# Optimization experiments

Measured on AMD Instinct MI355X. Metric: run time of the kernel, lower is better.

The kernel has to match this reference:

```python
import jax, jax.numpy as jnp
import numpy as np

N = 100_000   # nodes
E = 3_200_000 # edges (avg degree 32)
IN = 256      # input feature dim


def setup_inputs() -> dict:
    key = jax.random.key(0)
    ks = jax.random.split(key, 10)
    w = lambda k, s: (jax.random.normal(k, s, jnp.float32) * 0.02)
    return {
        "x": jax.random.normal(ks[0], (N, IN), jnp.float32),
        "edge_index": jax.random.randint(ks[1], (2, E), 0, N, dtype=jnp.int32),
        "edge_attr": jax.random.normal(ks[2], (E, 1), jnp.float32),
        # conv1: ExpGraphConv(IN, 64, 128)
        "W1a": w(ks[3], (IN, 64)), "b1a": jnp.zeros((64,), jnp.float32),
        "W1b": w(ks[4], (IN + 64, 128)), "b1b": jnp.zeros((128,), jnp.float32),
        # conv2: ExpGraphConv(128, 32->hidden 64? per ctor (128, 32, 64)): msg hidden 32... kept as repo: hidden=32? Using (128,64) msg, (192,64) out per faithful cat structure
        "W2a": w(ks[5], (128, 64)), "b2a": jnp.zeros((64,), jnp.float32),
        "W2b": w(ks[6], (128 + 64, 64)), "b2b": jnp.zeros((64,), jnp.float32),
        # head
        "Wl1": w(ks[7], (64, 32)), "bl1": jnp.zeros((32,), jnp.float32),
        "Wl2": w(ks[8], (32, 1)), "bl2": jnp.zeros((1,), jnp.float32),
    }


def _mean_aggr(h, src, dst, n):
    # gather messages from source nodes, scatter-mean into destination nodes
    s = jax.ops.segment_sum(h[src], dst, num_segments=n)          # [N, d]
    cnt = jax.ops.segment_sum(jnp.ones((src.shape[0],), h.dtype), dst, num_segments=n)
    return s / jnp.maximum(cnt, 1.0)[:, None]


def _exp_graph_conv(x, src, dst, Wa, ba, Wb, bb):
    # message MLP on source features, mean aggregation, then linear on [x || aggr]
    h = x @ Wa + ba                                               # [N, hidden]
    m = _mean_aggr(h, src, dst, x.shape[0])                       # [N, hidden]
    return jnp.concatenate([x, m], axis=1) @ Wb + bb              # [N, out]


def reference(x, edge_index, edge_attr, W1a, b1a, W1b, b1b, W2a, b2a, W2b, b2b, Wl1, bl1, Wl2, bl2):
    src, dst = edge_index[0], edge_index[1]
    x = jax.nn.relu(_exp_graph_conv(x, src, dst, W1a, b1a, W1b, b1b))
    x = jax.nn.relu(_exp_graph_conv(x, src, dst, W2a, b2a, W2b, b2b))
    x = jax.nn.relu(x @ Wl1 + bl1)
    return x @ Wl2 + bl2
```

## Files before the change

### kernel.cpp

```cpp
#include <hip/hip_runtime.h>

#define IN_DIM 256
#define CAP 10240
#define EPB 4096

typedef _Float16 f16;
typedef _Float16 f16x8 __attribute__((ext_vector_type(8)));
typedef float f32x4 __attribute__((ext_vector_type(4)));
typedef unsigned u32x4 __attribute__((ext_vector_type(4)));
typedef unsigned u32x2 __attribute__((ext_vector_type(2)));


__global__ __launch_bounds__(256) void bucket_scatter_k(const int* __restrict__ srcp,
                                                        const int* __restrict__ dstp,
                                                        int* __restrict__ bcur,
                                                        unsigned* __restrict__ bedge, int E) {
    __shared__ int cnt[512], lstart[512], delta[512], fill[512];
    __shared__ int pfx[256];
    __shared__ unsigned spay[EPB];
    __shared__ unsigned char sbk[EPB];
    int tid = threadIdx.x;
    cnt[tid] = 0; cnt[tid + 256] = 0;
    fill[tid] = 0; fill[tid + 256] = 0;
    __syncthreads();
    size_t base = (size_t)blockIdx.x * EPB;
    int nloc = E - (int)base; if (nloc > EPB) nloc = EPB;
    int dreg[EPB / 256], sreg[EPB / 256];
#pragma unroll
    for (int j = 0; j < EPB / 256; j++) {
        int e = j * 256 + tid;
        if (e < nloc) {
            dreg[j] = dstp[base + e];
            sreg[j] = srcp[base + e];
            atomicAdd(&cnt[dreg[j] >> 8], 1);
        }
    }
    __syncthreads();
    int a0 = cnt[2 * tid], a1 = cnt[2 * tid + 1], s = a0 + a1;
    pfx[tid] = s;
    __syncthreads();
    for (int off = 1; off < 256; off <<= 1) {
        int t2 = (tid >= off) ? pfx[tid - off] : 0;
        __syncthreads();
        pfx[tid] += t2;
        __syncthreads();
    }
    int excl = pfx[tid] - s;
    lstart[2 * tid] = excl;
    lstart[2 * tid + 1] = excl + a0;
    int g0 = 0, g1 = 0;
    if (a0) g0 = atomicAdd(&bcur[2 * tid], a0);
    if (a1) g1 = atomicAdd(&bcur[2 * tid + 1], a1);
    delta[2 * tid]     = (2 * tid) * CAP + g0 - excl;
    delta[2 * tid + 1] = (2 * tid + 1) * CAP + g1 - (excl + a0);
    __syncthreads();
#pragma unroll
    for (int j = 0; j < EPB / 256; j++) {
        int e = j * 256 + tid;
        if (e < nloc) {
            int d = dreg[j], bk = d >> 8;
            int slot = lstart[bk] + atomicAdd(&fill[bk], 1);
            spay[slot] = (unsigned)sreg[j] | ((unsigned)(d & 255) << 17);
            sbk[slot] = (unsigned char)bk;
        }
    }
    __syncthreads();
    int mid = lstart[256];
#pragma unroll
    for (int j = 0; j < EPB / 256; j++) {
        int i = j * 256 + tid;
        if (i < nloc) {
            int bk = (int)sbk[i] | ((i >= mid) ? 256 : 0);
            int gp = i + delta[bk];
            if (gp < (bk + 1) * CAP)
                bedge[gp] = spay[i];
        }
    }
}

__global__ __launch_bounds__(256) void fine_sort_k(unsigned* __restrict__ bedge,
                                                   const int* __restrict__ bcur,
                                                   int2* __restrict__ ose, int Nn) {
    __shared__ int cnt[256], cur[256], pfx[256];
    __shared__ int sorted[CAP];
    int b = blockIdx.x, tid = threadIdx.x;
    int lo = b * CAP;
    int sz = bcur[b];
    if (sz > CAP) sz = CAP;
    cnt[tid] = 0;
    __syncthreads();
    for (int i = tid; i < sz; i += 256) atomicAdd(&cnt[bedge[lo + i] >> 17], 1);
    __syncthreads();
    int c = cnt[tid];
    pfx[tid] = c;
    __syncthreads();
    for (int off = 1; off < 256; off <<= 1) {
        int t2 = (tid >= off) ? pfx[tid - off] : 0;
        __syncthreads();
        pfx[tid] += t2;
        __syncthreads();
    }
    int excl = pfx[tid] - c;
    cur[tid] = excl;
    int node = b * 256 + tid;
    if (node < Nn) ose[node] = make_int2(lo + excl, lo + excl + c);
    __syncthreads();
    for (int i = tid; i < sz; i += 256) {
        unsigned v = bedge[lo + i];
        int slot = atomicAdd(&cur[v >> 17], 1);
        sorted[slot] = (int)(v & 0x1FFFFu);
    }
    __syncthreads();
    for (int i = tid; i < sz; i += 256) bedge[lo + i] = (unsigned)sorted[i];
}


__global__ __launch_bounds__(256) void wcast_all_k(
    const float* __restrict__ W1a, const float* __restrict__ W1b,
    const float* __restrict__ W2a, const float* __restrict__ W2b,
    const float* __restrict__ b1a, const float* __restrict__ b1b,
    const float* __restrict__ b2a, const float* __restrict__ b2b,
    f16* __restrict__ Wt1, f16* __restrict__ Wt2,
    f16* __restrict__ Wmt1, f16* __restrict__ Wmt2,
    float* __restrict__ bc1, float* __restrict__ bc2) {
    int i = blockIdx.x * 256 + threadIdx.x;
    if (i < 49152) {
        int n = i >> 8, k = i & 255;
        Wt1[i] = (f16)(n < 64 ? W1a[k * 64 + n] : W1b[k * 128 + (n - 64)]);
    } else if (i < 65536) {
        int l = i - 49152; int n = l >> 7, k = l & 127;
        Wt2[l] = (f16)(n < 64 ? W2a[k * 64 + n] : W2b[k * 64 + (n - 64)]);
    } else if (i < 73728) {
        int l = i - 65536; int n = l >> 6, k = l & 63;
        Wmt1[l] = (f16)W1b[(256 + k) * 128 + n];
    } else if (i < 77824) {
        int l = i - 73728; int n = l >> 6, k = l & 63;
        Wmt2[l] = (f16)W2b[(128 + k) * 64 + n];
    } else if (i < 78016) {
        int l = i - 77824; bc1[l] = l < 64 ? b1a[l] : b1b[l - 64];
    } else if (i < 78144) {
        int l = i - 78016; bc2[l] = l < 64 ? b2a[l] : b2b[l - 64];
    }
}


template <int BN, bool A1F32>
__global__ __launch_bounds__(256) void gemm_fused(const void* __restrict__ A1v, int K1,
                                                  const f16* __restrict__ Wt,
                                                  const float* __restrict__ bc,
                                                  f16* __restrict__ Y1,
                                                  f16* __restrict__ Y2, int M) {
    constexpr int BM = 64, BK = 32, ASTR = BK + 8;
    constexpr int WN = BN / 2, NB = WN / 16, SEGB = BN / 64;
    constexpr int EPS = BN + 8, TPR = BN / 8, N2 = BN - 64;
    constexpr size_t SM_AB = (size_t)BM * ASTR * 2 + (size_t)BN * ASTR * 2;
    constexpr size_t SM_EP = (size_t)BM * EPS * 2;
    constexpr size_t SM = SM_AB > SM_EP ? SM_AB : SM_EP;
    __shared__ __align__(16) char smem[SM];
    f16* As = reinterpret_cast<f16*>(smem);
    f16* Bs = reinterpret_cast<f16*>(smem + (size_t)BM * ASTR * 2);
    const int tid  = threadIdx.x;
    const int wave = tid >> 6, lane = tid & 63;
    const int wr = wave >> 1, wc = wave & 1;
    const int quad = lane >> 4, l16 = lane & 15;
    const int row0 = blockIdx.x * BM;

    f32x4 acc[2][NB];
#pragma unroll
    for (int i = 0; i < 2; i++)
#pragma unroll
        for (int j = 0; j < NB; j++) acc[i][j] = (f32x4)(0.f);

    const int ra = tid >> 2, sa = tid & 3;
    int rowA = row0 + ra;  if (rowA >= M) rowA = M - 1;

    u32x4 aReg, bReg[SEGB];
    auto loadA = [&](int kk) {
        if constexpr (A1F32) {
            const float* bp = reinterpret_cast<const float*>(A1v) +
                              (size_t)rowA * K1 + kk + sa * 8;
            f32x4 v0 = __builtin_nontemporal_load(reinterpret_cast<const f32x4*>(bp));
            f32x4 v1 = __builtin_nontemporal_load(reinterpret_cast<const f32x4*>(bp) + 1);
            union { f16 h[8]; u32x4 u; } p;
            p.h[0] = (f16)v0.x; p.h[1] = (f16)v0.y; p.h[2] = (f16)v0.z; p.h[3] = (f16)v0.w;
            p.h[4] = (f16)v1.x; p.h[5] = (f16)v1.y; p.h[6] = (f16)v1.z; p.h[7] = (f16)v1.w;
            aReg = p.u;
        } else {
            aReg = __builtin_nontemporal_load(reinterpret_cast<const u32x4*>(
                reinterpret_cast<const f16*>(A1v) + (size_t)rowA * K1 + kk + sa * 8));
        }
    };
    auto loadB = [&](int kk) {
#pragma unroll
        for (int i = 0; i < SEGB; i++) {
            int fid = tid + i * 256;
            int n = fid >> 2, s = fid & 3;
            bReg[i] = *reinterpret_cast<const u32x4*>(Wt + (size_t)n * K1 + kk + s * 8);
        }
    };

    loadA(0); loadB(0);
    for (int kk = 0; kk < K1; kk += BK) {
        *reinterpret_cast<u32x4*>(&As[ra * ASTR + sa * 8]) = aReg;
#pragma unroll
        for (int i = 0; i < SEGB; i++) {
            int fid = tid + i * 256;
            int n = fid >> 2, s = fid & 3;
            *reinterpret_cast<u32x4*>(&Bs[n * ASTR + s * 8]) = bReg[i];
        }
        __syncthreads();
        if (kk + BK < K1) { loadA(kk + BK); loadB(kk + BK); }
        f16x8 af[2], bf[NB];
#pragma unroll
        for (int rb = 0; rb < 2; rb++) {
            int row = wr * 32 + rb * 16 + l16;
            af[rb] = *reinterpret_cast<const f16x8*>(&As[row * ASTR + quad * 8]);
        }
#pragma unroll
        for (int cb = 0; cb < NB; cb++) {
            int n = wc * WN + cb * 16 + l16;
            bf[cb] = *reinterpret_cast<const f16x8*>(&Bs[n * ASTR + quad * 8]);
        }
#pragma unroll
        for (int rb = 0; rb < 2; rb++)
#pragma unroll
            for (int cb = 0; cb < NB; cb++)
                acc[rb][cb] = __builtin_amdgcn_mfma_f32_16x16x32_f16(af[rb], bf[cb], acc[rb][cb], 0, 0, 0);
        __syncthreads();
    }

    f16* ep = reinterpret_cast<f16*>(smem);
#pragma unroll
    for (int rb = 0; rb < 2; rb++) {
#pragma unroll
        for (int cb = 0; cb < NB; cb++) {
            int col = wc * WN + cb * 16 + l16;
            float bv = bc[col];
#pragma unroll
            for (int r = 0; r < 4; r++) {
                int lrow = wr * 32 + rb * 16 + quad * 4 + r;
                ep[(size_t)lrow * EPS + col] = (f16)(acc[rb][cb][r] + bv);
            }
        }
    }
    __syncthreads();
#pragma unroll
    for (int p = 0; p < BM * TPR / 256; p++) {
        int fid = p * 256 + tid;
        int row = fid / TPR, c = fid % TPR, col0 = c * 8;
        int grow = row0 + row;
        if (grow < M) {
            u32x4 val = *reinterpret_cast<const u32x4*>(&ep[(size_t)row * EPS + col0]);
            if (col0 < 64)
                *reinterpret_cast<u32x4*>(Y1 + (size_t)grow * 64 + col0) = val;
            else
                __builtin_nontemporal_store(val,
                    reinterpret_cast<u32x4*>(Y2 + (size_t)grow * N2 + (col0 - 64)));
        }
    }
}


__global__ __launch_bounds__(256) void aggr_k(const int2* __restrict__ ose,
                                              const int* __restrict__ ssrc,
                                              const f16* __restrict__ h,
                                              f16* __restrict__ m, int n) {
    int wave = (blockIdx.x * 256 + threadIdx.x) >> 6;
    int lane = threadIdx.x & 63;
    if (wave >= n) return;
    int2 se = ose[wave];
    int s0 = se.x, s1 = se.y;
    int q = lane >> 4, l16 = lane & 15;
    const u32x2* hp = reinterpret_cast<const u32x2*>(h);
    float a0 = 0.f, a1 = 0.f, a2 = 0.f, a3 = 0.f;
    auto acc = [&](u32x2 u) {
        union { u32x2 u; f16 hh[4]; } p; p.u = u;
        a0 += (float)p.hh[0]; a1 += (float)p.hh[1];
        a2 += (float)p.hh[2]; a3 += (float)p.hh[3];
    };
    for (int c = s0; c < s1; c += 64) {
        int cn = min(64, s1 - c);
        int myidx = (lane < cn) ? ssrc[c + lane] : 0;
        int t = 0;
        for (; t + 16 <= cn; t += 16) {
            int ia = __shfl(myidx, t + q);
            int ib = __shfl(myidx, t + 4 + q);
            int ic = __shfl(myidx, t + 8 + q);
            int id = __shfl(myidx, t + 12 + q);
            u32x2 ua = hp[(size_t)ia * 16 + l16];
            u32x2 ub = hp[(size_t)ib * 16 + l16];
            u32x2 uc = hp[(size_t)ic * 16 + l16];
            u32x2 ud = hp[(size_t)id * 16 + l16];
            acc(ua); acc(ub); acc(uc); acc(ud);
        }
        for (; t < cn; t += 4) {
            int r = t + q;
            int rr = (r < cn) ? r : (cn - 1);
            int ia = __shfl(myidx, rr);
            if (r < cn) acc(hp[(size_t)ia * 16 + l16]);
        }
    }
    a0 += __shfl_xor(a0, 16); a1 += __shfl_xor(a1, 16);
    a2 += __shfl_xor(a2, 16); a3 += __shfl_xor(a3, 16);
    a0 += __shfl_xor(a0, 32); a1 += __shfl_xor(a1, 32);
    a2 += __shfl_xor(a2, 32); a3 += __shfl_xor(a3, 32);
    if (lane < 16) {
        float inv = 1.0f / fmaxf((float)(s1 - s0), 1.0f);
        union { u32x2 u; f16 hh[4]; } p;
        p.hh[0] = (f16)(a0 * inv); p.hh[1] = (f16)(a1 * inv);
        p.hh[2] = (f16)(a2 * inv); p.hh[3] = (f16)(a3 * inv);
        reinterpret_cast<u32x2*>(m + (size_t)wave * 64)[l16] = p.u;
    }
}


template <int BN, bool HEAD>
__global__ __launch_bounds__(256) void combine_k(const f16* __restrict__ Mb,
                                                 const f16* __restrict__ Wmt,
                                                 const f16* __restrict__ P,
                                                 f16* __restrict__ Y,
                                                 const float* __restrict__ Wl1,
                                                 const float* __restrict__ bl1,
                                                 const float* __restrict__ Wl2,
                                                 const float* __restrict__ bl2,
                                                 float* __restrict__ out, int M) {
    constexpr int BM = 64, ASTR = 72;
    constexpr int WN = BN / 2, NB = WN / 16;
    constexpr int EPS = BN + 8, TPR = BN / 8;
    constexpr size_t SZ_A = (size_t)BM * ASTR * 2;
    constexpr size_t SM_AB = SZ_A + (size_t)BN * ASTR * 2;
    constexpr size_t SM_EP = (size_t)BM * EPS * 2;
    constexpr size_t SM_CORE = SM_AB > SM_EP ? SM_AB : SM_EP;
    constexpr size_t SM_HEAD = HEAD ? (2048 + 64) * 4 : 0;
    __shared__ __align__(16) char smem[SM_CORE + SM_HEAD];
    f16* As = reinterpret_cast<f16*>(smem);
    f16* Bs = reinterpret_cast<f16*>(smem + SZ_A);
    const int tid  = threadIdx.x;
    const int wave = tid >> 6, lane = tid & 63;
    const int wr = wave >> 1, wc = wave & 1;
    const int quad = lane >> 4, l16 = lane & 15;
    const int row0 = blockIdx.x * BM;

#pragma unroll
    for (int fid = tid; fid < 512; fid += 256) {
        int row = fid >> 3, s = fid & 7;
        int grow = row0 + row; if (grow >= M) grow = M - 1;
        *reinterpret_cast<u32x4*>(&As[row * ASTR + s * 8]) =
            *reinterpret_cast<const u32x4*>(Mb + (size_t)grow * 64 + s * 8);
    }
    for (int fid = tid; fid < BN * 8; fid += 256) {
        int n = fid >> 3, s = fid & 7;
        *reinterpret_cast<u32x4*>(&Bs[n * ASTR + s * 8]) =
            *reinterpret_cast<const u32x4*>(Wmt + (size_t)n * 64 + s * 8);
    }
    if constexpr (HEAD) {
        float* w1s = reinterpret_cast<float*>(smem + SM_CORE);
        for (int t2 = tid; t2 < 2048; t2 += 256) w1s[t2] = Wl1[t2];
        if (tid < 32) { w1s[2048 + tid] = bl1[tid]; w1s[2048 + 32 + tid] = Wl2[tid]; }
    }
    __syncthreads();

    f32x4 acc[2][NB];
#pragma unroll
    for (int i = 0; i < 2; i++)
#pragma unroll
        for (int j = 0; j < NB; j++) acc[i][j] = (f32x4)(0.f);
#pragma unroll
    for (int ks = 0; ks < 2; ks++) {
        f16x8 af[2], bf[NB];
#pragma unroll
        for (int rb = 0; rb < 2; rb++) {
            int row = wr * 32 + rb * 16 + l16;
            af[rb] = *reinterpret_cast<const f16x8*>(&As[row * ASTR + ks * 32 + quad * 8]);
        }
#pragma unroll
        for (int cb = 0; cb < NB; cb++) {
            int n = wc * WN + cb * 16 + l16;
            bf[cb] = *reinterpret_cast<const f16x8*>(&Bs[n * ASTR + ks * 32 + quad * 8]);
        }
#pragma unroll
        for (int rb = 0; rb < 2; rb++)
#pragma unroll
            for (int cb = 0; cb < NB; cb++)
                acc[rb][cb] = __builtin_amdgcn_mfma_f32_16x16x32_f16(af[rb], bf[cb], acc[rb][cb], 0, 0, 0);
    }
    __syncthreads();

    f16* ep = reinterpret_cast<f16*>(smem);
#pragma unroll
    for (int rb = 0; rb < 2; rb++) {
#pragma unroll
        for (int cb = 0; cb < NB; cb++) {
            int col = wc * WN + cb * 16 + l16;
#pragma unroll
            for (int r = 0; r < 4; r++) {
                int lrow = wr * 32 + rb * 16 + quad * 4 + r;
                int grow = row0 + lrow;
                float pv = (grow < M) ? (float)P[(size_t)grow * BN + col] : 0.f;
                float v = fmaxf(acc[rb][cb][r] + pv, 0.f);
                ep[(size_t)lrow * EPS + col] = (f16)v;
            }
        }
    }
    __syncthreads();

    if constexpr (HEAD) {
        float* w1s = reinterpret_cast<float*>(smem + SM_CORE);
        float* b1s = w1s + 2048;
        float* w2s = b1s + 32;
        int row = tid >> 2, part = tid & 3;
        const f16* eprow = ep + (size_t)row * EPS;
        float hj[8];
#pragma unroll
        for (int j = 0; j < 8; j++) hj[j] = b1s[part * 8 + j];
        for (int k = 0; k < 64; k++) {
            float v = (float)eprow[k];
            const float* wrow = &w1s[k * 32 + part * 8];
#pragma unroll
            for (int j = 0; j < 8; j++) hj[j] += v * wrow[j];
        }
        float o = 0.f;
#pragma unroll
        for (int j = 0; j < 8; j++) o += fmaxf(hj[j], 0.f) * w2s[part * 8 + j];
        o += __shfl_xor(o, 1);
        o += __shfl_xor(o, 2);
        int grow = row0 + row;
        if (part == 0 && grow < M) out[grow] = o + bl2[0];
    } else {
#pragma unroll
        for (int p = 0; p < BM * TPR / 256; p++) {
            int fid = p * 256 + tid;
            int row = fid / TPR, c = fid % TPR;
            int grow = row0 + row;
            if (grow < M) {
                u32x4 val = *reinterpret_cast<const u32x4*>(&ep[(size_t)row * EPS + c * 8]);
                *reinterpret_cast<u32x4*>(Y + (size_t)grow * BN + c * 8) = val;
            }
        }
    }
}


extern "C" void kernel_launch(void* const* d_in, const int* in_sizes, int n_in,
                              void* d_out, int out_size, void* d_ws, size_t ws_size,
                              hipStream_t stream) {
    const float* x   = (const float*)d_in[0];
    const int*   ei  = (const int*)d_in[1];
    const float* W1a = (const float*)d_in[3];
    const float* b1a = (const float*)d_in[4];
    const float* W1b = (const float*)d_in[5];
    const float* b1b = (const float*)d_in[6];
    const float* W2a = (const float*)d_in[7];
    const float* b2a = (const float*)d_in[8];
    const float* W2b = (const float*)d_in[9];
    const float* b2b = (const float*)d_in[10];
    const float* Wl1 = (const float*)d_in[11];
    const float* bl1 = (const float*)d_in[12];
    const float* Wl2 = (const float*)d_in[13];
    const float* bl2 = (const float*)d_in[14];

    const int N = in_sizes[0] / IN_DIM;
    const int E = in_sizes[1] / 2;
    const int* srcp = ei;
    const int* dstp = ei + E;

    char* ws = (char*)d_ws;
    size_t off = 0;
    auto alloc = [&](size_t bytes) -> char* {
        char* p = ws + off;
        off = (off + bytes + 255) & ~(size_t)255;
        return p;
    };
    int NB2 = (N + 255) / 256;
    int*      bcur  = (int*)alloc(512 * 4);
    unsigned* bedge = (unsigned*)alloc((size_t)NB2 * CAP * 4);
    int2*     ose   = (int2*)alloc((size_t)N * 8);
    f16*      hbuf  = (f16*)alloc((size_t)N * 64 * 2);
    f16*      mbuf  = (f16*)alloc((size_t)N * 64 * 2);
    f16*      pbuf  = (f16*)alloc((size_t)N * 128 * 2);
    f16*      x1    = (f16*)alloc((size_t)N * 128 * 2);
    f16*      h2    = (f16*)alloc((size_t)N * 64 * 2);
    f16*      p2    = (f16*)alloc((size_t)N * 64 * 2);
    f16*      Wt1   = (f16*)alloc(192 * 256 * 2);
    f16*      Wt2   = (f16*)alloc(128 * 128 * 2);
    f16*      Wmt1  = (f16*)alloc(128 * 64 * 2);
    f16*      Wmt2  = (f16*)alloc(64 * 64 * 2);
    float*    bc1   = (float*)alloc(192 * 4);
    float*    bc2   = (float*)alloc(128 * 4);
    (void)ws_size;

    hipMemsetAsync(bcur, 0, 512 * 4, stream);
    int ebk = (E + EPB - 1) / EPB;
    bucket_scatter_k<<<ebk, 256, 0, stream>>>(srcp, dstp, bcur, bedge, E);
    fine_sort_k<<<NB2, 256, 0, stream>>>(bedge, bcur, ose, N);

    wcast_all_k<<<306, 256, 0, stream>>>(W1a, W1b, W2a, W2b, b1a, b1b, b2a, b2b,
                                         Wt1, Wt2, Wmt1, Wmt2, bc1, bc2);

    int mb = (N + 63) / 64;
    int ab = (N * 64 + 255) / 256;
    const int* ssrc = (const int*)bedge;

    gemm_fused<192, true><<<mb, 256, 0, stream>>>(x, 256, Wt1, bc1, hbuf, pbuf, N);
    aggr_k<<<ab, 256, 0, stream>>>(ose, ssrc, hbuf, mbuf, N);
    combine_k<128, false><<<mb, 256, 0, stream>>>(mbuf, Wmt1, pbuf, x1,
                                                  nullptr, nullptr, nullptr, nullptr,
                                                  nullptr, N);

    gemm_fused<128, false><<<mb, 256, 0, stream>>>(x1, 128, Wt2, bc2, h2, p2, N);
    aggr_k<<<ab, 256, 0, stream>>>(ose, ssrc, h2, mbuf, N);
    combine_k<64, true><<<mb, 256, 0, stream>>>(mbuf, Wmt2, p2, nullptr,
                                                Wl1, bl1, Wl2, bl2, (float*)d_out, N);
}
```

Baseline: 445.9 us.

## Fuse layer-1 combine with layer-2 GEMM and slice hidden features for aggregation

Layer-1 combine and the layer-2 projection GEMM now run in one kernel, so the x1 intermediate never round-trips through global memory. Hidden features h are stored in four 16-column slices, and aggregation runs per slice via a 2D grid, so each gather reads a 32-byte segment that is more likely to stay cache-resident. The bcur memset is folded into the weight-cast prep kernel. The trade-offs are four times as many index loads and shuffles in aggregation, and more shared memory and register pressure in the fused kernel.

```diff
diff --git a/kernel.cpp b/kernel.cpp
--- a/kernel.cpp
+++ b/kernel.cpp
@@ -115,15 +115,18 @@
 }
 
 
-__global__ __launch_bounds__(256) void wcast_all_k(
+__global__ __launch_bounds__(256) void prep_k(
     const float* __restrict__ W1a, const float* __restrict__ W1b,
     const float* __restrict__ W2a, const float* __restrict__ W2b,
     const float* __restrict__ b1a, const float* __restrict__ b1b,
     const float* __restrict__ b2a, const float* __restrict__ b2b,
     f16* __restrict__ Wt1, f16* __restrict__ Wt2,
     f16* __restrict__ Wmt1, f16* __restrict__ Wmt2,
-    float* __restrict__ bc1, float* __restrict__ bc2) {
-    int i = blockIdx.x * 256 + threadIdx.x;
+    float* __restrict__ bc1, float* __restrict__ bc2,
+    int* __restrict__ bcur) {
+    int tid = threadIdx.x;
+    if (blockIdx.x == 0) { bcur[tid] = 0; bcur[tid + 256] = 0; }
+    int i = blockIdx.x * 256 + tid;
     if (i < 49152) {
         int n = i >> 8, k = i & 255;
         Wt1[i] = (f16)(n < 64 ? W1a[k * 64 + n] : W1b[k * 128 + (n - 64)]);
@@ -144,15 +147,14 @@
 }
 
 
-template <int BN, bool A1F32>
-__global__ __launch_bounds__(256) void gemm_fused(const void* __restrict__ A1v, int K1,
-                                                  const f16* __restrict__ Wt,
-                                                  const float* __restrict__ bc,
-                                                  f16* __restrict__ Y1,
-                                                  f16* __restrict__ Y2, int M) {
-    constexpr int BM = 64, BK = 32, ASTR = BK + 8;
+__global__ __launch_bounds__(256) void gemm_fused192(const float* __restrict__ A1,
+                                                     const f16* __restrict__ Wt,
+                                                     const float* __restrict__ bc,
+                                                     f16* __restrict__ Y1,
+                                                     f16* __restrict__ Y2, int M) {
+    constexpr int BN = 192, BM = 64, BK = 32, ASTR = BK + 8, K1 = 256;
     constexpr int WN = BN / 2, NB = WN / 16, SEGB = BN / 64;
-    constexpr int EPS = BN + 8, TPR = BN / 8, N2 = BN - 64;
+    constexpr int EPS = BN + 8, TPR = BN / 8;
     constexpr size_t SM_AB = (size_t)BM * ASTR * 2 + (size_t)BN * ASTR * 2;
     constexpr size_t SM_EP = (size_t)BM * EPS * 2;
     constexpr size_t SM = SM_AB > SM_EP ? SM_AB : SM_EP;
@@ -176,19 +178,13 @@
 
     u32x4 aReg, bReg[SEGB];
     auto loadA = [&](int kk) {
-        if constexpr (A1F32) {
-            const float* bp = reinterpret_cast<const float*>(A1v) +
-                              (size_t)rowA * K1 + kk + sa * 8;
-            f32x4 v0 = __builtin_nontemporal_load(reinterpret_cast<const f32x4*>(bp));
-            f32x4 v1 = __builtin_nontemporal_load(reinterpret_cast<const f32x4*>(bp) + 1);
-            union { f16 h[8]; u32x4 u; } p;
-            p.h[0] = (f16)v0.x; p.h[1] = (f16)v0.y; p.h[2] = (f16)v0.z; p.h[3] = (f16)v0.w;
-            p.h[4] = (f16)v1.x; p.h[5] = (f16)v1.y; p.h[6] = (f16)v1.z; p.h[7] = (f16)v1.w;
-            aReg = p.u;
-        } else {
-            aReg = __builtin_nontemporal_load(reinterpret_cast<const u32x4*>(
-                reinterpret_cast<const f16*>(A1v) + (size_t)rowA * K1 + kk + sa * 8));
-        }
+        const float* bp = A1 + (size_t)rowA * K1 + kk + sa * 8;
+        f32x4 v0 = __builtin_nontemporal_load(reinterpret_cast<const f32x4*>(bp));
+        f32x4 v1 = __builtin_nontemporal_load(reinterpret_cast<const f32x4*>(bp) + 1);
+        union { f16 h[8]; u32x4 u; } p;
+        p.h[0] = (f16)v0.x; p.h[1] = (f16)v0.y; p.h[2] = (f16)v0.z; p.h[3] = (f16)v0.w;
+        p.h[4] = (f16)v1.x; p.h[5] = (f16)v1.y; p.h[6] = (f16)v1.z; p.h[7] = (f16)v1.w;
+        aReg = p.u;
     };
     auto loadB = [&](int kk) {
 #pragma unroll
@@ -251,11 +247,13 @@
         int grow = row0 + row;
         if (grow < M) {
             u32x4 val = *reinterpret_cast<const u32x4*>(&ep[(size_t)row * EPS + col0]);
-            if (col0 < 64)
-                *reinterpret_cast<u32x4*>(Y1 + (size_t)grow * 64 + col0) = val;
-            else
+            if (col0 < 64) {
+                f16* dst = Y1 + (size_t)(col0 >> 4) * M * 16 + (size_t)grow * 16 + (col0 & 15);
+                *reinterpret_cast<u32x4*>(dst) = val;
+            } else {
                 __builtin_nontemporal_store(val,
-                    reinterpret_cast<u32x4*>(Y2 + (size_t)grow * N2 + (col0 - 64)));
+                    reinterpret_cast<u32x4*>(Y2 + (size_t)grow * 128 + (col0 - 64)));
+            }
         }
     }
 }
@@ -265,15 +263,16 @@
                                               const int* __restrict__ ssrc,
                                               const f16* __restrict__ h,
                                               f16* __restrict__ m, int n) {
-    int wave = (blockIdx.x * 256 + threadIdx.x) >> 6;
-    int lane = threadIdx.x & 63;
-    if (wave >= n) return;
-    int2 se = ose[wave];
+    const int slice = blockIdx.y;
+    const int node = blockIdx.x * 4 + (threadIdx.x >> 6);
+    const int lane = threadIdx.x & 63;
+    if (node >= n) return;
+    int2 se = ose[node];
     int s0 = se.x, s1 = se.y;
-    int q = lane >> 4, l16 = lane & 15;
-    const u32x2* hp = reinterpret_cast<const u32x2*>(h);
+    const int l4 = lane & 3, r16 = lane >> 2;
+    const u32x2* hp = reinterpret_cast<const u32x2*>(h + (size_t)slice * n * 16);
     float a0 = 0.f, a1 = 0.f, a2 = 0.f, a3 = 0.f;
-    auto acc = [&](u32x2 u) {
+    auto accum = [&](u32x2 u) {
         union { u32x2 u; f16 hh[4]; } p; p.u = u;
         a0 += (float)p.hh[0]; a1 += (float)p.hh[1];
         a2 += (float)p.hh[2]; a3 += (float)p.hh[3];
@@ -282,57 +281,212 @@
         int cn = min(64, s1 - c);
         int myidx = (lane < cn) ? ssrc[c + lane] : 0;
         int t = 0;
-        for (; t + 16 <= cn; t += 16) {
-            int ia = __shfl(myidx, t + q);
-            int ib = __shfl(myidx, t + 4 + q);
-            int ic = __shfl(myidx, t + 8 + q);
-            int id = __shfl(myidx, t + 12 + q);
-            u32x2 ua = hp[(size_t)ia * 16 + l16];
-            u32x2 ub = hp[(size_t)ib * 16 + l16];
-            u32x2 uc = hp[(size_t)ic * 16 + l16];
-            u32x2 ud = hp[(size_t)id * 16 + l16];
-            acc(ua); acc(ub); acc(uc); acc(ud);
-        }
-        for (; t < cn; t += 4) {
-            int r = t + q;
+        for (; t + 32 <= cn; t += 32) {
+            int ia = __shfl(myidx, t + r16);
+            int ib = __shfl(myidx, t + 16 + r16);
+            u32x2 ua = hp[(size_t)ia * 4 + l4];
+            u32x2 ub = hp[(size_t)ib * 4 + l4];
+            accum(ua); accum(ub);
+        }
+        if (t + 16 <= cn) {
+            int ia = __shfl(myidx, t + r16);
+            accum(hp[(size_t)ia * 4 + l4]);
+            t += 16;
+        }
+        if (t < cn) {
+            int r = t + r16;
             int rr = (r < cn) ? r : (cn - 1);
             int ia = __shfl(myidx, rr);
-            if (r < cn) acc(hp[(size_t)ia * 16 + l16]);
-        }
-    }
-    a0 += __shfl_xor(a0, 16); a1 += __shfl_xor(a1, 16);
-    a2 += __shfl_xor(a2, 16); a3 += __shfl_xor(a3, 16);
-    a0 += __shfl_xor(a0, 32); a1 += __shfl_xor(a1, 32);
-    a2 += __shfl_xor(a2, 32); a3 += __shfl_xor(a3, 32);
-    if (lane < 16) {
+            if (r < cn) accum(hp[(size_t)ia * 4 + l4]);
+        }
+    }
+    a0 += __shfl_xor(a0, 4);  a1 += __shfl_xor(a1, 4);  a2 += __shfl_xor(a2, 4);  a3 += __shfl_xor(a3, 4);
+    a0 += __shfl_xor(a0, 8);  a1 += __shfl_xor(a1, 8);  a2 += __shfl_xor(a2, 8);  a3 += __shfl_xor(a3, 8);
+    a0 += __shfl_xor(a0, 16); a1 += __shfl_xor(a1, 16); a2 += __shfl_xor(a2, 16); a3 += __shfl_xor(a3, 16);
+    a0 += __shfl_xor(a0, 32); a1 += __shfl_xor(a1, 32); a2 += __shfl_xor(a2, 32); a3 += __shfl_xor(a3, 32);
+    if (lane < 4) {
         float inv = 1.0f / fmaxf((float)(s1 - s0), 1.0f);
-        union { u32x2 u; f16 hh[4]; } p;
-        p.hh[0] = (f16)(a0 * inv); p.hh[1] = (f16)(a1 * inv);
-        p.hh[2] = (f16)(a2 * inv); p.hh[3] = (f16)(a3 * inv);
-        reinterpret_cast<u32x2*>(m + (size_t)wave * 64)[l16] = p.u;
-    }
-}
-
-
-template <int BN, bool HEAD>
-__global__ __launch_bounds__(256) void combine_k(const f16* __restrict__ Mb,
-                                                 const f16* __restrict__ Wmt,
-                                                 const f16* __restrict__ P,
-                                                 f16* __restrict__ Y,
-                                                 const float* __restrict__ Wl1,
-                                                 const float* __restrict__ bl1,
-                                                 const float* __restrict__ Wl2,
-                                                 const float* __restrict__ bl2,
-                                                 float* __restrict__ out, int M) {
-    constexpr int BM = 64, ASTR = 72;
-    constexpr int WN = BN / 2, NB = WN / 16;
-    constexpr int EPS = BN + 8, TPR = BN / 8;
+        union { u32x2 u; f16 hh[4]; } pk;
+        pk.hh[0] = (f16)(a0 * inv); pk.hh[1] = (f16)(a1 * inv);
+        pk.hh[2] = (f16)(a2 * inv); pk.hh[3] = (f16)(a3 * inv);
+        u32x2* mp = reinterpret_cast<u32x2*>(m + (size_t)slice * n * 16 + (size_t)node * 16);
+        mp[l4] = pk.u;
+    }
+}
+
+
+__global__ __launch_bounds__(256) void comb_gemm_k(const f16* __restrict__ Mb,
+                                                   const f16* __restrict__ Wmt,
+                                                   const f16* __restrict__ P,
+                                                   const f16* __restrict__ Wt2,
+                                                   const float* __restrict__ bc2,
+                                                   f16* __restrict__ H2,
+                                                   f16* __restrict__ P2,
+                                                   int M) {
+    constexpr int BM = 64, ASTR = 72, TSTR = 136, BSTR = 40;
+    constexpr int BN1 = 128, NB1 = 4;
+    constexpr int BN2 = 128, NB2c = 4;
+    __shared__ __align__(16) char smem[27648];
+    f16* As  = reinterpret_cast<f16*>(smem);
+    f16* Bs1 = reinterpret_cast<f16*>(smem + (size_t)BM * ASTR * 2);
+    f16* tile = reinterpret_cast<f16*>(smem);
+    f16* Bs2 = reinterpret_cast<f16*>(smem + (size_t)BM * TSTR * 2);
+    const int tid  = threadIdx.x;
+    const int wave = tid >> 6, lane = tid & 63;
+    const int wr = wave >> 1, wc = wave & 1;
+    const int quad = lane >> 4, l16 = lane & 15;
+    const int row0 = blockIdx.x * BM;
+
+#pragma unroll
+    for (int fid = tid; fid < 512; fid += 256) {
+        int row = fid >> 3, s = fid & 7;
+        int grow = row0 + row; if (grow >= M) grow = M - 1;
+        const f16* src = Mb + (size_t)(s >> 1) * M * 16 + (size_t)grow * 16 + (s & 1) * 8;
+        *reinterpret_cast<u32x4*>(&As[row * ASTR + s * 8]) =
+            *reinterpret_cast<const u32x4*>(src);
+    }
+#pragma unroll
+    for (int fid = tid; fid < BN1 * 8; fid += 256) {
+        int n = fid >> 3, s = fid & 7;
+        *reinterpret_cast<u32x4*>(&Bs1[n * ASTR + s * 8]) =
+            *reinterpret_cast<const u32x4*>(Wmt + (size_t)n * 64 + s * 8);
+    }
+    __syncthreads();
+
+    f32x4 acc[2][NB1];
+#pragma unroll
+    for (int i = 0; i < 2; i++)
+#pragma unroll
+        for (int j = 0; j < NB1; j++) acc[i][j] = (f32x4)(0.f);
+#pragma unroll
+    for (int ks = 0; ks < 2; ks++) {
+        f16x8 af[2], bf[NB1];
+#pragma unroll
+        for (int rb = 0; rb < 2; rb++) {
+            int row = wr * 32 + rb * 16 + l16;
+            af[rb] = *reinterpret_cast<const f16x8*>(&As[row * ASTR + ks * 32 + quad * 8]);
+        }
+#pragma unroll
+        for (int cb = 0; cb < NB1; cb++) {
+            int n = wc * 64 + cb * 16 + l16;
+            bf[cb] = *reinterpret_cast<const f16x8*>(&Bs1[n * ASTR + ks * 32 + quad * 8]);
+        }
+#pragma unroll
+        for (int rb = 0; rb < 2; rb++)
+#pragma unroll
+            for (int cb = 0; cb < NB1; cb++)
+                acc[rb][cb] = __builtin_amdgcn_mfma_f32_16x16x32_f16(af[rb], bf[cb], acc[rb][cb], 0, 0, 0);
+    }
+    __syncthreads();
+
+#pragma unroll
+    for (int rb = 0; rb < 2; rb++) {
+#pragma unroll
+        for (int cb = 0; cb < NB1; cb++) {
+            int col = wc * 64 + cb * 16 + l16;
+#pragma unroll
+            for (int r = 0; r < 4; r++) {
+                int lrow = wr * 32 + rb * 16 + quad * 4 + r;
+                int grow = row0 + lrow;
+                float pv = (grow < M) ? (float)P[(size_t)grow * 128 + col] : 0.f;
+                tile[(size_t)lrow * TSTR + col] = (f16)fmaxf(acc[rb][cb][r] + pv, 0.f);
+            }
+        }
+    }
+
+    f32x4 acc2[2][NB2c];
+#pragma unroll
+    for (int i = 0; i < 2; i++)
+#pragma unroll
+        for (int j = 0; j < NB2c; j++) acc2[i][j] = (f32x4)(0.f);
+
+    u32x4 bReg[2];
+    auto loadB2 = [&](int kk) {
+#pragma unroll
+        for (int i = 0; i < 2; i++) {
+            int fid = tid + i * 256;
+            int n = fid >> 2, s = fid & 3;
+            bReg[i] = *reinterpret_cast<const u32x4*>(Wt2 + (size_t)n * 128 + kk + s * 8);
+        }
+    };
+    loadB2(0);
+    for (int kk = 0; kk < 128; kk += 32) {
+#pragma unroll
+        for (int i = 0; i < 2; i++) {
+            int fid = tid + i * 256;
+            int n = fid >> 2, s = fid & 3;
+            *reinterpret_cast<u32x4*>(&Bs2[n * BSTR + s * 8]) = bReg[i];
+        }
+        __syncthreads();
+        if (kk + 32 < 128) loadB2(kk + 32);
+        f16x8 af[2], bf[NB2c];
+#pragma unroll
+        for (int rb = 0; rb < 2; rb++) {
+            int row = wr * 32 + rb * 16 + l16;
+            af[rb] = *reinterpret_cast<const f16x8*>(&tile[(size_t)row * TSTR + kk + quad * 8]);
+        }
+#pragma unroll
+        for (int cb = 0; cb < NB2c; cb++) {
+            int n = wc * 64 + cb * 16 + l16;
+            bf[cb] = *reinterpret_cast<const f16x8*>(&Bs2[n * BSTR + quad * 8]);
+        }
+#pragma unroll
+        for (int rb = 0; rb < 2; rb++)
+#pragma unroll
+            for (int cb = 0; cb < NB2c; cb++)
+                acc2[rb][cb] = __builtin_amdgcn_mfma_f32_16x16x32_f16(af[rb], bf[cb], acc2[rb][cb], 0, 0, 0);
+        __syncthreads();
+    }
+
+    f16* ep = tile;
+#pragma unroll
+    for (int rb = 0; rb < 2; rb++) {
+#pragma unroll
+        for (int cb = 0; cb < NB2c; cb++) {
+            int col = wc * 64 + cb * 16 + l16;
+            float bv = bc2[col];
+#pragma unroll
+            for (int r = 0; r < 4; r++) {
+                int lrow = wr * 32 + rb * 16 + quad * 4 + r;
+                ep[(size_t)lrow * TSTR + col] = (f16)(acc2[rb][cb][r] + bv);
+            }
+        }
+    }
+    __syncthreads();
+#pragma unroll
+    for (int p = 0; p < 4; p++) {
+        int fid = p * 256 + tid;
+        int row = fid >> 4, c = fid & 15, col0 = c * 8;
+        int grow = row0 + row;
+        if (grow < M) {
+            u32x4 val = *reinterpret_cast<const u32x4*>(&ep[(size_t)row * TSTR + col0]);
+            if (col0 < 64) {
+                f16* dst = H2 + (size_t)(col0 >> 4) * M * 16 + (size_t)grow * 16 + (col0 & 15);
+                *reinterpret_cast<u32x4*>(dst) = val;
+            } else {
+                __builtin_nontemporal_store(val,
+                    reinterpret_cast<u32x4*>(P2 + (size_t)grow * 64 + (col0 - 64)));
+            }
+        }
+    }
+}
+
+
+__global__ __launch_bounds__(256) void comb_head_k(const f16* __restrict__ Mb,
+                                                   const f16* __restrict__ Wmt,
+                                                   const f16* __restrict__ P,
+                                                   const float* __restrict__ Wl1,
+                                                   const float* __restrict__ bl1,
+                                                   const float* __restrict__ Wl2,
+                                                   const float* __restrict__ bl2,
+                                                   float* __restrict__ out, int M) {
+    constexpr int BM = 64, ASTR = 72, BN = 64, NB = 2;
+    constexpr int EPS = BN + 8;
     constexpr size_t SZ_A = (size_t)BM * ASTR * 2;
     constexpr size_t SM_AB = SZ_A + (size_t)BN * ASTR * 2;
     constexpr size_t SM_EP = (size_t)BM * EPS * 2;
     constexpr size_t SM_CORE = SM_AB > SM_EP ? SM_AB : SM_EP;
-    constexpr size_t SM_HEAD = HEAD ? (2048 + 64) * 4 : 0;
-    __shared__ __align__(16) char smem[SM_CORE + SM_HEAD];
+    __shared__ __align__(16) char smem[SM_CORE + (2048 + 64) * 4];
     f16* As = reinterpret_cast<f16*>(smem);
     f16* Bs = reinterpret_cast<f16*>(smem + SZ_A);
     const int tid  = threadIdx.x;
@@ -345,15 +499,16 @@
     for (int fid = tid; fid < 512; fid += 256) {
         int row = fid >> 3, s = fid & 7;
         int grow = row0 + row; if (grow >= M) grow = M - 1;
+        const f16* src = Mb + (size_t)(s >> 1) * M * 16 + (size_t)grow * 16 + (s & 1) * 8;
         *reinterpret_cast<u32x4*>(&As[row * ASTR + s * 8]) =
-            *reinterpret_cast<const u32x4*>(Mb + (size_t)grow * 64 + s * 8);
+            *reinterpret_cast<const u32x4*>(src);
     }
     for (int fid = tid; fid < BN * 8; fid += 256) {
         int n = fid >> 3, s = fid & 7;
         *reinterpret_cast<u32x4*>(&Bs[n * ASTR + s * 8]) =
             *reinterpret_cast<const u32x4*>(Wmt + (size_t)n * 64 + s * 8);
     }
-    if constexpr (HEAD) {
+    {
         float* w1s = reinterpret_cast<float*>(smem + SM_CORE);
         for (int t2 = tid; t2 < 2048; t2 += 256) w1s[t2] = Wl1[t2];
         if (tid < 32) { w1s[2048 + tid] = bl1[tid]; w1s[2048 + 32 + tid] = Wl2[tid]; }
@@ -375,7 +530,7 @@
         }
 #pragma unroll
         for (int cb = 0; cb < NB; cb++) {
-            int n = wc * WN + cb * 16 + l16;
+            int n = wc * 32 + cb * 16 + l16;
             bf[cb] = *reinterpret_cast<const f16x8*>(&Bs[n * ASTR + ks * 32 + quad * 8]);
         }
 #pragma unroll
@@ -391,53 +546,39 @@
     for (int rb = 0; rb < 2; rb++) {
 #pragma unroll
         for (int cb = 0; cb < NB; cb++) {
-            int col = wc * WN + cb * 16 + l16;
+            int col = wc * 32 + cb * 16 + l16;
 #pragma unroll
             for (int r = 0; r < 4; r++) {
                 int lrow = wr * 32 + rb * 16 + quad * 4 + r;
                 int grow = row0 + lrow;
-                float pv = (grow < M) ? (float)P[(size_t)grow * BN + col] : 0.f;
-                float v = fmaxf(acc[rb][cb][r] + pv, 0.f);
-                ep[(size_t)lrow * EPS + col] = (f16)v;
+                float pv = (grow < M) ? (float)P[(size_t)grow * 64 + col] : 0.f;
+                ep[(size_t)lrow * EPS + col] = (f16)fmaxf(acc[rb][cb][r] + pv, 0.f);
             }
         }
     }
     __syncthreads();
 
-    if constexpr (HEAD) {
-        float* w1s = reinterpret_cast<float*>(smem + SM_CORE);
-        float* b1s = w1s + 2048;
-        float* w2s = b1s + 32;
-        int row = tid >> 2, part = tid & 3;
-        const f16* eprow = ep + (size_t)row * EPS;
-        float hj[8];
-#pragma unroll
-        for (int j = 0; j < 8; j++) hj[j] = b1s[part * 8 + j];
-        for (int k = 0; k < 64; k++) {
-            float v = (float)eprow[k];
-            const float* wrow = &w1s[k * 32 + part * 8];
-#pragma unroll
-            for (int j = 0; j < 8; j++) hj[j] += v * wrow[j];
-        }
-        float o = 0.f;
-#pragma unroll
-        for (int j = 0; j < 8; j++) o += fmaxf(hj[j], 0.f) * w2s[part * 8 + j];
-        o += __shfl_xor(o, 1);
-        o += __shfl_xor(o, 2);
-        int grow = row0 + row;
-        if (part == 0 && grow < M) out[grow] = o + bl2[0];
-    } else {
-#pragma unroll
-        for (int p = 0; p < BM * TPR / 256; p++) {
-            int fid = p * 256 + tid;
-            int row = fid / TPR, c = fid % TPR;
-            int grow = row0 + row;
-            if (grow < M) {
-                u32x4 val = *reinterpret_cast<const u32x4*>(&ep[(size_t)row * EPS + c * 8]);
-                *reinterpret_cast<u32x4*>(Y + (size_t)grow * BN + c * 8) = val;
-            }
-        }
-    }
+    float* w1s = reinterpret_cast<float*>(smem + SM_CORE);
+    float* b1s = w1s + 2048;
+    float* w2s = b1s + 32;
+    int row = tid >> 2, part = tid & 3;
+    const f16* eprow = ep + (size_t)row * EPS;
+    float hj[8];
+#pragma unroll
+    for (int j = 0; j < 8; j++) hj[j] = b1s[part * 8 + j];
+    for (int k = 0; k < 64; k++) {
+        float v = (float)eprow[k];
+        const float* wrow = &w1s[k * 32 + part * 8];
+#pragma unroll
+        for (int j = 0; j < 8; j++) hj[j] += v * wrow[j];
+    }
+    float o = 0.f;
+#pragma unroll
+    for (int j = 0; j < 8; j++) o += fmaxf(hj[j], 0.f) * w2s[part * 8 + j];
+    o += __shfl_xor(o, 1);
+    o += __shfl_xor(o, 2);
+    int grow = row0 + row;
+    if (part == 0 && grow < M) out[grow] = o + bl2[0];
 }
 
 
@@ -478,7 +619,6 @@
     f16*      hbuf  = (f16*)alloc((size_t)N * 64 * 2);
     f16*      mbuf  = (f16*)alloc((size_t)N * 64 * 2);
     f16*      pbuf  = (f16*)alloc((size_t)N * 128 * 2);
-    f16*      x1    = (f16*)alloc((size_t)N * 128 * 2);
     f16*      h2    = (f16*)alloc((size_t)N * 64 * 2);
     f16*      p2    = (f16*)alloc((size_t)N * 64 * 2);
     f16*      Wt1   = (f16*)alloc(192 * 256 * 2);
@@ -489,26 +629,21 @@
     float*    bc2   = (float*)alloc(128 * 4);
     (void)ws_size;
 
-    hipMemsetAsync(bcur, 0, 512 * 4, stream);
+    prep_k<<<306, 256, 0, stream>>>(W1a, W1b, W2a, W2b, b1a, b1b, b2a, b2b,
+                                    Wt1, Wt2, Wmt1, Wmt2, bc1, bc2, bcur);
     int ebk = (E + EPB - 1) / EPB;
     bucket_scatter_k<<<ebk, 256, 0, stream>>>(srcp, dstp, bcur, bedge, E);
     fine_sort_k<<<NB2, 256, 0, stream>>>(bedge, bcur, ose, N);
 
-    wcast_all_k<<<306, 256, 0, stream>>>(W1a, W1b, W2a, W2b, b1a, b1b, b2a, b2b,
-                                         Wt1, Wt2, Wmt1, Wmt2, bc1, bc2);
-
     int mb = (N + 63) / 64;
-    int ab = (N * 64 + 255) / 256;
+    dim3 ag((N + 3) / 4, 4);
     const int* ssrc = (const int*)bedge;
 
-    gemm_fused<192, true><<<mb, 256, 0, stream>>>(x, 256, Wt1, bc1, hbuf, pbuf, N);
-    aggr_k<<<ab, 256, 0, stream>>>(ose, ssrc, hbuf, mbuf, N);
-    combine_k<128, false><<<mb, 256, 0, stream>>>(mbuf, Wmt1, pbuf, x1,
-                                                  nullptr, nullptr, nullptr, nullptr,
-                                                  nullptr, N);
-
-    gemm_fused<128, false><<<mb, 256, 0, stream>>>(x1, 128, Wt2, bc2, h2, p2, N);
-    aggr_k<<<ab, 256, 0, stream>>>(ose, ssrc, h2, mbuf, N);
-    combine_k<64, true><<<mb, 256, 0, stream>>>(mbuf, Wmt2, p2, nullptr,
-                                                Wl1, bl1, Wl2, bl2, (float*)d_out, N);
-}
+    gemm_fused192<<<mb, 256, 0, stream>>>(x, Wt1, bc1, hbuf, pbuf, N);
+    aggr_k<<<ag, 256, 0, stream>>>(ose, ssrc, hbuf, mbuf, N);
+    comb_gemm_k<<<mb, 256, 0, stream>>>(mbuf, Wmt1, pbuf, Wt2, bc2, h2, p2, N);
+
+    aggr_k<<<ag, 256, 0, stream>>>(ose, ssrc, h2, mbuf, N);
+    comb_head_k<<<mb, 256, 0, stream>>>(mbuf, Wmt2, p2, Wl1, bl1, Wl2, bl2,
+                                        (float*)d_out, N);
+}
```

After: 561.3 us. 1.26x slower.
